# Kernel tuning notes

Measured on AMD Instinct MI355X. Metric: run time of the kernel, lower is better.

## Reference

```python
import jax, jax.numpy as jnp
import numpy as np

B, N_C, N_T, D, DF = 16, 2048, 1024, 2, 2
K, E_OBS = 16, 4
H, DH = 4, 16
F = H * DH  # 64-dim node features (embed_all output)


def setup_inputs() -> dict:
    key = jax.random.key(0)
    ks = jax.random.split(key, 16)
    r = lambda i, shape: jax.random.normal(ks[i], shape, jnp.float32) * 0.05
    d_in = E_OBS + D + DF  # obs(4) + s(2) + f(2) = 8
    return dict(
        s_ctx=jax.random.normal(ks[0], (B, N_C, D), jnp.float32),
        f_ctx=jax.random.normal(ks[1], (B, N_C, DF), jnp.float32),
        s_test=jax.random.normal(ks[2], (B, N_T, D), jnp.float32),
        emb_obs=r(3, (2, E_OBS)),
        W1=r(4, (d_in, 256)), b1=jnp.zeros((256,), jnp.float32),
        W2=r(5, (256, 128)), b2=jnp.zeros((128,), jnp.float32),
        W3=r(6, (128, F)), b3=jnp.zeros((F,), jnp.float32),
        ln_g=jnp.ones((F,), jnp.float32), ln_b=jnp.zeros((F,), jnp.float32),
        Wg=r(7, (F, F)),
        a_src=r(8, (H, DH)), a_dst=r(9, (H, DH)),
        We=r(10, (D, H)), be=jnp.zeros((H,), jnp.float32),
        H1=r(11, (F, 256)), c1=jnp.zeros((256,), jnp.float32),
        H2=r(12, (256, 64)), c2=jnp.zeros((64,), jnp.float32),
        H3=r(13, (64, 2)), c3=jnp.zeros((2,), jnp.float32),
    )


def _knn(q, ctx, k):
    # q [B,Nq,D], ctx [B,Nc,D] -> neighbor indices [B,Nq,K] and displacement edge feats [B,Nq,K,D]
    d2 = (jnp.sum(q * q, -1)[:, :, None] + jnp.sum(ctx * ctx, -1)[:, None, :]
          - 2.0 * jnp.einsum('bqd,bcd->bqc', q, ctx))
    _, idx = jax.lax.top_k(-d2, k)
    nb = jax.vmap(lambda c, i: c[i])(ctx, idx)  # gather neighbor coords per batch
    return idx, q[:, :, None, :] - nb


def _mlp3(x, W1, b1, W2, b2, W3, b3):
    x = jax.nn.gelu(x @ W1 + b1)
    x = jax.nn.gelu(x @ W2 + b2)
    return x @ W3 + b3


def _ln(x, g, b):
    mu = jnp.mean(x, -1, keepdims=True)
    v = jnp.var(x, -1, keepdims=True)
    return (x - mu) * jax.lax.rsqrt(v + 1e-6) * g + b


def reference(s_ctx, f_ctx, s_test, emb_obs, W1, b1, W2, b2, W3, b3, ln_g, ln_b,
              Wg, a_src, a_dst, We, be, H1, c1, H2, c2, H3, c3):
    # --- build kNN graph (ctx->ctx and ctx->test edges, K per receiver) ---
    s_cc, d_cc = _knn(s_ctx, s_ctx, K)
    s_ct, d_ct = _knn(s_test, s_ctx, K)
    edges = jnp.concatenate([d_cc.reshape(-1, D), d_ct.reshape(-1, D)], axis=0)  # [E, D]
    off = (jnp.arange(B) * N_C)[:, None, None]
    senders = jnp.concatenate([(s_cc + off).reshape(-1), (s_ct + off).reshape(-1)])  # [E]
    # receivers == repeat(arange(N), K): edges are grouped K-per-node in node order.

    # --- node embedding: [obs_embed | s | f] -> MLP -> LayerNorm ---
    ctx_in = jnp.concatenate([jnp.broadcast_to(emb_obs[1], (B, N_C, E_OBS)), s_ctx, f_ctx], -1)
    test_in = jnp.concatenate([jnp.broadcast_to(emb_obs[0], (B, N_T, E_OBS)), s_test,
                               jnp.zeros((B, N_T, DF), s_test.dtype)], -1)
    n_ctx = _ln(_mlp3(ctx_in, W1, b1, W2, b2, W3, b3), ln_g, ln_b)
    n_test = _ln(_mlp3(test_in, W1, b1, W2, b2, W3, b3), ln_g, ln_b)
    nodes = jnp.concatenate([n_ctx.reshape(B * N_C, F), n_test.reshape(B * N_T, F)], 0)
    N = B * (N_C + N_T)

    # --- edge-biased GAT message passing (K incoming edges per node) ---
    xp = (nodes @ Wg).reshape(N, H, DH)
    msg = xp[senders].reshape(N, K, H, DH)  # gather sender features
    sc = (jnp.einsum('nkhd,hd->nkh', msg, a_src)
          + jnp.einsum('nhd,hd->nh', xp, a_dst)[:, None, :])
    sc = jax.nn.leaky_relu(sc, 0.2) + (edges @ We + be).reshape(N, K, H)  # edge bias
    alpha = jax.nn.softmax(sc, axis=1)  # softmax over the K neighbors
    out = jnp.einsum('nkh,nkhd->nhd', alpha, msg).reshape(N, F)
    nodes = nodes + out  # residual

    # --- head on test nodes + diagonal MVN output ---
    n_t = nodes[-B * N_T:].reshape(B, N_T, F)
    o = jax.nn.gelu(n_t @ H1 + c1)
    o = jax.nn.gelu(o @ H2 + c2)
    o = o @ H3 + c3  # [B, N_t, 2]
    mean = o[..., 0:1]
    scale = jax.nn.softplus(o[..., 1:2])
    return jnp.concatenate([mean, scale], -1)
```

## Files before the change

### kernel.cpp

```cpp
#include <hip/hip_runtime.h>
#include <math.h>

#define NB 16
#define NCTX 2048
#define NTEST 1024
#define NCTX_TOT (NB*NCTX)
#define NTEST_TOT (NB*NTEST)
#define NTOT (NCTX_TOT + NTEST_TOT)

typedef _Float16 half8 __attribute__((ext_vector_type(8)));
typedef _Float16 half4 __attribute__((ext_vector_type(4)));
typedef float f32x4 __attribute__((ext_vector_type(4)));

__device__ __forceinline__ float gelu_f(float x) {
  float x3 = x * x * x;
  float y = 0.7978845608028654f * fmaf(0.044715f, x3, x);
  float e = __expf(2.0f * y);
  float th = 1.0f - 2.0f * __builtin_amdgcn_rcpf(e + 1.0f);
  return 0.5f * x * (1.0f + th);
}

__device__ __forceinline__ void fma4(float4& a, float s, float4 w) {
  a.x = fmaf(s, w.x, a.x);
  a.y = fmaf(s, w.y, a.y);
  a.z = fmaf(s, w.z, a.z);
  a.w = fmaf(s, w.w, a.w);
}

__device__ __forceinline__ float4 ldg4(const float* p) {
  return *reinterpret_cast<const float4*>(p);
}

__device__ __forceinline__ unsigned fkey(float f) {
  unsigned u = __float_as_uint(f);
  return (u & 0x80000000u) ? ~u : (u ^ 0x80000000u);
}
__device__ __forceinline__ float unfkey(unsigned k) {
  return (k & 0x80000000u) ? __uint_as_float(k ^ 0x80000000u)
                           : __uint_as_float(~k);
}

__global__ __launch_bounds__(256, 3) void knn_prep_kernel(
    const float* __restrict__ s_ctx, const float* __restrict__ s_test,
    int* __restrict__ senders,
    const float* __restrict__ W1, const float* __restrict__ b1,
    const float* __restrict__ emb,
    const float* __restrict__ W2, const float* __restrict__ W3,
    const float* __restrict__ Wg,
    const float* __restrict__ H1, const float* __restrict__ H2,
    _Float16* __restrict__ W2P, _Float16* __restrict__ W3P,
    _Float16* __restrict__ WgP,
    _Float16* __restrict__ H1P, _Float16* __restrict__ H2P,
    float* __restrict__ ctype)
{
  __shared__ __align__(16) unsigned long long sk[4][128];
  const int blk = blockIdx.x;

  if (blk < 40) {
    const int t = blk*256 + (int)threadIdx.x;
    if (t < 4096) {
      int i = t;
      int j = i >> 9, ks = (i >> 6) & 7, l = i & 63;
      int col = 16*j + (l & 15);
      int k0  = ks*32 + (l >> 4)*8;
      half8 o;
      #pragma unroll
      for (int e = 0; e < 8; ++e) o[e] = (_Float16)W2[(k0 + e)*128 + col];
      *reinterpret_cast<half8*>(&W2P[(size_t)i*8]) = o;
    } else if (t < 5120) {
      int i = t - 4096;
      int j = i >> 8, ks = (i >> 6) & 3, l = i & 63;
      int col = 16*j + (l & 15);
      int k0  = ks*32 + (l >> 4)*8;
      half8 o;
      #pragma unroll
      for (int e = 0; e < 8; ++e) o[e] = (_Float16)W3[(k0 + e)*64 + col];
      *reinterpret_cast<half8*>(&W3P[(size_t)i*8]) = o;
    } else if (t < 5632) {
      int i = t - 5120;
      int j = i >> 7, ks = (i >> 6) & 1, l = i & 63;
      int col = 16*j + (l & 15);
      int k0  = ks*32 + (l >> 4)*8;
      half8 o;
      #pragma unroll
      for (int e = 0; e < 8; ++e) o[e] = (_Float16)Wg[(k0 + e)*64 + col];
      *reinterpret_cast<half8*>(&WgP[(size_t)i*8]) = o;
    } else if (t < 7680) {
      int i = t - 5632;
      int j = i >> 7, ks = (i >> 6) & 1, l = i & 63;
      int col = 16*j + (l & 15);
      int k0  = ks*32 + (l >> 4)*8;
      half8 o;
      #pragma unroll
      for (int e = 0; e < 8; ++e) o[e] = (_Float16)H1[(k0 + e)*256 + col];
      *reinterpret_cast<half8*>(&H1P[(size_t)i*8]) = o;
    } else if (t < 9728) {
      int i = t - 7680;
      int j = i >> 9, ks = (i >> 6) & 7, l = i & 63;
      int col = 16*j + (l & 15);
      int k0  = ks*32 + (l >> 4)*8;
      half8 o;
      #pragma unroll
      for (int e = 0; e < 8; ++e) o[e] = (_Float16)H2[(k0 + e)*64 + col];
      *reinterpret_cast<half8*>(&H2P[(size_t)i*8]) = o;
    } else {
      int i = t - 9728;
      int ty = i >> 8, c = i & 255;
      float acc = b1[c];
      #pragma unroll
      for (int k = 0; k < 4; ++k) acc = fmaf(emb[ty*4 + k], W1[k*256 + c], acc);
      ctype[i] = acc;
    }
    return;
  }

  const int t    = threadIdx.x;
  const int lane = t & 63;
  const int w    = t >> 6;
  const int b0   = blk - 40;
  const int unit = (b0 & 7)*512 + (b0 >> 3);
  const int bb   = unit >> 8;
  const int q    = (unit & 255) * 4 + w;
  const int trow = bb * NTEST + q;

  const float* cb = s_ctx + (size_t)bb * NCTX * 2;
  const float qx = s_test[(size_t)trow*2];
  const float qy = s_test[(size_t)trow*2 + 1];
  const float qq = __fadd_rn(__fmul_rn(qx,qx), __fmul_rn(qy,qy));

  float2 p[32];
  #pragma unroll
  for (int it = 0; it < 32; ++it)
    p[it] = *reinterpret_cast<const float2*>(&cb[2*(it*64 + lane)]);

  float d[32];
  float mn = 3.4e38f;
  #pragma unroll
  for (int it = 0; it < 32; ++it) {
    float ss  = __fadd_rn(__fmul_rn(p[it].x,p[it].x), __fmul_rn(p[it].y,p[it].y));
    float dot = __fadd_rn(__fmul_rn(qx, p[it].x), __fmul_rn(qy, p[it].y));
    float d2  = __fsub_rn(__fadd_rn(qq, ss), __fmul_rn(2.0f, dot));
    d[it] = d2;
    mn = fminf(mn, d2);
  }

  unsigned v = fkey(mn);
  #pragma unroll
  for (int k = 2; k <= 64; k <<= 1) {
    #pragma unroll
    for (int j = k >> 1; j >= 1; j >>= 1) {
      unsigned pv = (unsigned)__shfl_xor((int)v, j);
      bool up      = ((lane & k) == 0);
      bool lowHalf = ((lane & j) == 0);
      bool keepMin = (lowHalf == up);
      unsigned mnv = v < pv ? v : pv;
      unsigned mxv = v < pv ? pv : v;
      v = keepMin ? mnv : mxv;
    }
  }
  const float Tf = unfkey((unsigned)__shfl((int)v, 15));

  int cnt = 0;
  #pragma unroll
  for (int it = 0; it < 32; ++it) cnt += (int)(d[it] <= Tf);
  int inc = cnt;
  #pragma unroll
  for (int o = 1; o < 64; o <<= 1) {
    int y = __shfl_up(inc, o);
    if (lane >= o) inc += y;
  }
  const int S = __shfl(inc, 63);
  int pos = inc - cnt;
  #pragma unroll
  for (int it = 0; it < 32; ++it) {
    if (d[it] <= Tf) {
      if (pos < 128)
        sk[w][pos] = ((unsigned long long)fkey(d[it]) << 32)
                   | (unsigned)(it*64 + lane);
      ++pos;
    }
  }

  if (S <= 32) {
    if (lane >= S && lane < 32) sk[w][lane] = ~0ULL;
    unsigned long long pm = sk[w][lane & 31];
    unsigned long long kv[32];
    #pragma unroll
    for (int j = 0; j < 32; ++j) kv[j] = sk[w][j];
    int r0 = 0;
    #pragma unroll
    for (int j = 0; j < 32; ++j)
      r0 += (int)(kv[j] < pm);
    if (lane < S && r0 < 16)
      senders[(size_t)trow*16 + r0] = bb*NCTX + (int)(pm & 0xFFFFFFFFu);
  } else if (S <= 128) {
    unsigned long long p0 = (lane      < S) ? sk[w][lane]      : ~0ULL;
    unsigned long long p1 = (lane + 64 < S) ? sk[w][lane + 64] : ~0ULL;
    int r0 = 0, r1 = 0;
    for (int j = 0; j < S; ++j) {
      unsigned long long kj = sk[w][j];
      r0 += (int)(kj < p0);
      r1 += (int)(kj < p1);
    }
    if (lane < S && r0 < 16)
      senders[(size_t)trow*16 + r0] = bb*NCTX + (int)(p0 & 0xFFFFFFFFu);
    if (lane + 64 < S && r1 < 16)
      senders[(size_t)trow*16 + r1] = bb*NCTX + (int)(p1 & 0xFFFFFFFFu);
  } else {
    if (lane == 0) {
      float dist[16]; int ind[16];
      #pragma unroll
      for (int j=0;j<16;++j){ dist[j]=3.4e38f; ind[j]=0; }
      for (int c = 0; c < NCTX; ++c) {
        float2 pp = *reinterpret_cast<const float2*>(&cb[2*c]);
        float ss  = __fadd_rn(__fmul_rn(pp.x,pp.x), __fmul_rn(pp.y,pp.y));
        float dot = __fadd_rn(__fmul_rn(qx, pp.x), __fmul_rn(qy, pp.y));
        float d2  = __fsub_rn(__fadd_rn(qq, ss), __fmul_rn(2.0f, dot));
        if (d2 < dist[15]) {
          float dj = d2; int ij = c;
          #pragma unroll
          for (int j = 0; j < 16; ++j) {
            bool sw = dj < dist[j];
            float td = dist[j]; int ti = ind[j];
            dist[j] = sw ? dj : td;  ind[j] = sw ? ij : ti;
            dj = sw ? td : dj;       ij = sw ? ti : ij;
          }
        }
      }
      for (int j = 0; j < 16; ++j)
        senders[(size_t)trow*16 + j] = bb*NCTX + ind[j];
    }
  }
}

__global__ __launch_bounds__(256, 4) void mlp_kernel(
    const float* __restrict__ s_ctx, const float* __restrict__ f_ctx,
    const float* __restrict__ s_test,
    const float* __restrict__ ctype, const float* __restrict__ W1,
    const _Float16* __restrict__ W2P, const float* __restrict__ b2,
    const _Float16* __restrict__ W3P, const float* __restrict__ b3,
    const float* __restrict__ ln_g, const float* __restrict__ ln_b,
    const _Float16* __restrict__ WgP,
    const float* __restrict__ a_src, const float* __restrict__ a_dst,
    float* __restrict__ nodes, _Float16* __restrict__ xph,
    float* __restrict__ xps, float* __restrict__ xpd)
{
  __shared__ __align__(16) char smem[34816];
  const int t    = threadIdx.x;
  const int lane = t & 63;
  const int w    = t >> 6;
  const int id   = blockIdx.x;
  char* slice = smem + w * 8704;
  _Float16* h1t  = reinterpret_cast<_Float16*>(slice);
  float (*xin)[4] = reinterpret_cast<float(*)[4]>(slice + 8448);
  _Float16* h2   = h1t;
  _Float16* nodh = h1t + 16*136;
  const int cn = lane & 15;
  const int kg = lane >> 4;
  const int m0 = (id*4 + w) * 16;
  const bool is_ctx = (m0 < NCTX_TOT);

  const _Float16* bQ2 = W2P + lane*8;
  const _Float16* bQ3 = W3P + lane*8;
  const _Float16* bQg = WgP + lane*8;

  half8 bb2[8];
  #pragma unroll
  for (int j = 0; j < 8; ++j)
    bb2[j] = *reinterpret_cast<const half8*>(bQ2 + j*4096);

  {
    int r = lane >> 2, c = lane & 3;
    int n = m0 + r;
    float v;
    if (is_ctx) v = (c < 2) ? s_ctx[2*(size_t)n + c] : f_ctx[2*(size_t)n + (c-2)];
    else { int tn = n - NCTX_TOT; v = (c < 2) ? s_test[2*(size_t)tn + c] : 0.f; }
    xin[r][c] = v;
  }

  {
    const int c0 = lane * 4;
    float4 w4 = ldg4(&W1[4*256 + c0]);
    float4 w5 = ldg4(&W1[5*256 + c0]);
    float4 w6 = ldg4(&W1[6*256 + c0]);
    float4 w7 = ldg4(&W1[7*256 + c0]);
    float4 cbv = ldg4(&ctype[(is_ctx ? 256 : 0) + c0]);
    #pragma unroll
    for (int r = 0; r < 16; ++r) {
      float4 xi = *reinterpret_cast<const float4*>(&xin[r][0]);
      float4 a = cbv;
      fma4(a, xi.x, w4); fma4(a, xi.y, w5);
      fma4(a, xi.z, w6); fma4(a, xi.w, w7);
      half4 o = { (_Float16)gelu_f(a.x), (_Float16)gelu_f(a.y),
                  (_Float16)gelu_f(a.z), (_Float16)gelu_f(a.w) };
      *reinterpret_cast<half4*>(&h1t[r*264 + c0]) = o;
    }
  }

  {
    f32x4 acc[8];
    #pragma unroll
    for (int j = 0; j < 8; ++j) {
      float bv = b2[16*j + cn];
      acc[j] = (f32x4){bv, bv, bv, bv};
    }
    const _Float16* aP = h1t + cn*264 + kg*8;
    #pragma unroll
    for (int ks = 0; ks < 8; ++ks) {
      half8 a = *reinterpret_cast<const half8*>(aP + ks*32);
      half8 bn[8];
      if (ks < 7) {
        #pragma unroll
        for (int j = 0; j < 8; ++j)
          bn[j] = *reinterpret_cast<const half8*>(bQ2 + j*4096 + (ks+1)*512);
      }
      #pragma unroll
      for (int j = 0; j < 8; ++j)
        acc[j] = __builtin_amdgcn_mfma_f32_16x16x32_f16(a, bb2[j], acc[j], 0, 0, 0);
      if (ks < 7) {
        #pragma unroll
        for (int j = 0; j < 8; ++j) bb2[j] = bn[j];
      }
    }
    #pragma unroll
    for (int j = 0; j < 8; ++j)
      #pragma unroll
      for (int r = 0; r < 4; ++r) {
        int m = kg*4 + r;
        h2[m*136 + 16*j + cn] = (_Float16)gelu_f(acc[j][r]);
      }
  }

  {
    f32x4 acc[4];
    #pragma unroll
    for (int j = 0; j < 4; ++j) {
      float bv = b3[16*j + cn];
      acc[j] = (f32x4){bv, bv, bv, bv};
    }
    const _Float16* aP = h2 + cn*136 + kg*8;
    half8 bb[4];
    #pragma unroll
    for (int j = 0; j < 4; ++j)
      bb[j] = *reinterpret_cast<const half8*>(bQ3 + j*2048);
    #pragma unroll
    for (int ks = 0; ks < 4; ++ks) {
      half8 a = *reinterpret_cast<const half8*>(aP + ks*32);
      half8 bn[4];
      if (ks < 3) {
        #pragma unroll
        for (int j = 0; j < 4; ++j)
          bn[j] = *reinterpret_cast<const half8*>(bQ3 + j*2048 + (ks+1)*512);
      }
      #pragma unroll
      for (int j = 0; j < 4; ++j)
        acc[j] = __builtin_amdgcn_mfma_f32_16x16x32_f16(a, bb[j], acc[j], 0, 0, 0);
      if (ks < 3) {
        #pragma unroll
        for (int j = 0; j < 4; ++j) bb[j] = bn[j];
      }
    }
    float gv[4], bvv[4];
    #pragma unroll
    for (int j = 0; j < 4; ++j) { gv[j] = ln_g[16*j+cn]; bvv[j] = ln_b[16*j+cn]; }
    const bool is_test = !is_ctx;
    #pragma unroll
    for (int r = 0; r < 4; ++r) {
      float sv = 0.f, sq = 0.f;
      #pragma unroll
      for (int j = 0; j < 4; ++j) {
        float v = acc[j][r];
        sv += v; sq += v*v;
      }
      #pragma unroll
      for (int o = 1; o < 16; o <<= 1) {
        sv += __shfl_xor(sv, o);
        sq += __shfl_xor(sq, o);
      }
      float mean = sv * (1.0f/64.0f);
      float var  = sq * (1.0f/64.0f) - mean*mean;
      float rstd = rsqrtf(var + 1e-6f);
      int m = kg*4 + r;
      #pragma unroll
      for (int j = 0; j < 4; ++j) {
        float v = (acc[j][r] - mean) * rstd * gv[j] + bvv[j];
        nodh[m*72 + 16*j + cn] = (_Float16)v;
        if (is_test)
          nodes[(size_t)(m0 + m)*64 + 16*j + cn] = v;
      }
    }
  }

  {
    f32x4 acc[4];
    #pragma unroll
    for (int j = 0; j < 4; ++j) acc[j] = (f32x4){0.f, 0.f, 0.f, 0.f};
    const _Float16* aP = nodh + cn*72 + kg*8;
    half8 bg0[4], bg1[4];
    #pragma unroll
    for (int j = 0; j < 4; ++j) {
      bg0[j] = *reinterpret_cast<const half8*>(bQg + j*1024);
      bg1[j] = *reinterpret_cast<const half8*>(bQg + j*1024 + 512);
    }
    half8 a0 = *reinterpret_cast<const half8*>(aP);
    half8 a1 = *reinterpret_cast<const half8*>(aP + 32);
    #pragma unroll
    for (int j = 0; j < 4; ++j)
      acc[j] = __builtin_amdgcn_mfma_f32_16x16x32_f16(a0, bg0[j], acc[j], 0, 0, 0);
    #pragma unroll
    for (int j = 0; j < 4; ++j)
      acc[j] = __builtin_amdgcn_mfma_f32_16x16x32_f16(a1, bg1[j], acc[j], 0, 0, 0);
    #pragma unroll
    for (int r = 0; r < 4; ++r) {
      int m = kg*4 + r;
      #pragma unroll
      for (int j = 0; j < 4; ++j)
        xph[(size_t)(m0 + m)*64 + 16*j + cn] = (_Float16)acc[j][r];
    }
    const float* av = is_ctx ? a_src : a_dst;
    float av0 = av[cn], av1 = av[16+cn], av2 = av[32+cn], av3 = av[48+cn];
    #pragma unroll
    for (int r = 0; r < 4; ++r) {
      float p0 = acc[0][r]*av0, p1 = acc[1][r]*av1;
      float p2 = acc[2][r]*av2, p3 = acc[3][r]*av3;
      #pragma unroll
      for (int o = 1; o < 16; o <<= 1) {
        p0 += __shfl_xor(p0, o); p1 += __shfl_xor(p1, o);
        p2 += __shfl_xor(p2, o); p3 += __shfl_xor(p3, o);
      }
      if (cn == 0) {
        int m = kg*4 + r;
        float4 v = make_float4(p0, p1, p2, p3);
        if (is_ctx)
          *reinterpret_cast<float4*>(&xps[(size_t)(m0 + m)*4]) = v;
        else
          *reinterpret_cast<float4*>(&xpd[(size_t)(m0 + m - NCTX_TOT)*4]) = v;
      }
    }
  }
}

__global__ __launch_bounds__(128, 3) void back_kernel(
    const float* __restrict__ s_ctx, const float* __restrict__ s_test,
    const _Float16* __restrict__ xph, const int* __restrict__ senders,
    const float* __restrict__ xps, const float* __restrict__ xpd,
    const float* __restrict__ We, const float* __restrict__ be,
    const float* __restrict__ nodes,
    const _Float16* __restrict__ H1P, const float* __restrict__ c1,
    const _Float16* __restrict__ H2P, const float* __restrict__ c2,
    const float* __restrict__ H3, const float* __restrict__ c3,
    float* __restrict__ outp)
{
  __shared__ __align__(16) _Float16 xinh[16*72];
  __shared__ __align__(16) _Float16 h1[16*264];
  __shared__ float pp[2][16][2];
  const int tid  = threadIdx.x;
  const int lane = tid & 63;
  const int wv   = tid >> 6;
  const int cn   = lane & 15;
  const int kg   = lane >> 4;
  const int bid  = blockIdx.x;
  const int L    = (bid & 7)*128 + (bid >> 3);
  const int row0 = L * 16;

  {
    const int h  = kg;
    const int kk = cn;
    const int hb = lane & 48;
    const float we0 = We[h], we1 = We[4+h], beh = be[h];
    for (int rr = 0; rr < 8; ++rr) {
      const int rl   = wv*8 + rr;
      const int trow = row0 + rl;
      int s = senders[(size_t)trow*16 + kk];
      s = (s < 0) ? 0 : ((s >= NCTX_TOT) ? NCTX_TOT - 1 : s);
      float pre = xps[(size_t)s*4 + h] + xpd[(size_t)trow*4 + h];
      float lr  = pre >= 0.f ? pre : 0.2f * pre;
      const float qx = s_test[(size_t)trow*2];
      const float qy = s_test[(size_t)trow*2 + 1];
      float ex = qx - s_ctx[(size_t)s*2];
      float ey = qy - s_ctx[(size_t)s*2 + 1];
      float sc = lr + fmaf(ex, we0, fmaf(ey, we1, beh));
      float mx = sc;
      #pragma unroll
      for (int o = 1; o < 16; o <<= 1) mx = fmaxf(mx, __shfl_xor(mx, o));
      float e = __expf(sc - mx);
      float sum = e;
      #pragma unroll
      for (int o = 1; o < 16; o <<= 1) sum += __shfl_xor(sum, o);
      float alpha = e / sum;
      float outv = 0.f;
      #pragma unroll
      for (int k = 0; k < 16; ++k) {
        int   sk = __shfl(s, k);
        float al = __shfl(alpha, hb + k);
        outv = fmaf(al, (float)xph[(size_t)sk*64 + lane], outv);
      }
      float xv = nodes[(size_t)(NCTX_TOT + trow)*64 + lane] + outv;
      xinh[rl*72 + lane] = (_Float16)xv;
    }
  }

  __syncthreads();

  {
    const _Float16* aP  = xinh + cn*72 + kg*8;
    const _Float16* bQ1 = H1P + lane*8;
    half8 a0 = *reinterpret_cast<const half8*>(aP);
    half8 a1 = *reinterpret_cast<const half8*>(aP + 32);
    const int g = wv;
    f32x4 acc[8];
    #pragma unroll
    for (int j = 0; j < 8; ++j) {
      float bv = c1[16*(g*8 + j) + cn];
      acc[j] = (f32x4){bv, bv, bv, bv};
    }
    half8 b0[8], b1[8];
    #pragma unroll
    for (int j = 0; j < 8; ++j) {
      b0[j] = *reinterpret_cast<const half8*>(bQ1 + ((g*8 + j)*2 + 0)*512);
      b1[j] = *reinterpret_cast<const half8*>(bQ1 + ((g*8 + j)*2 + 1)*512);
    }
    #pragma unroll
    for (int j = 0; j < 8; ++j)
      acc[j] = __builtin_amdgcn_mfma_f32_16x16x32_f16(a0, b0[j], acc[j], 0, 0, 0);
    #pragma unroll
    for (int j = 0; j < 8; ++j)
      acc[j] = __builtin_amdgcn_mfma_f32_16x16x32_f16(a1, b1[j], acc[j], 0, 0, 0);
    #pragma unroll
    for (int j = 0; j < 8; ++j)
      #pragma unroll
      for (int r = 0; r < 4; ++r)
        h1[(kg*4 + r)*264 + 16*(g*8 + j) + cn] = (_Float16)gelu_f(acc[j][r]);
  }

  __syncthreads();

  {
    f32x4 acc[2];
    #pragma unroll
    for (int j2 = 0; j2 < 2; ++j2) {
      const int j = wv*2 + j2;
      float bv = c2[16*j + cn];
      acc[j2] = (f32x4){bv, bv, bv, bv};
    }
    const _Float16* aP  = h1 + cn*264 + kg*8;
    const _Float16* bQ2 = H2P + lane*8;
    half8 bb[2];
    #pragma unroll
    for (int j2 = 0; j2 < 2; ++j2)
      bb[j2] = *reinterpret_cast<const half8*>(bQ2 + (wv*2 + j2)*4096);
    #pragma unroll
    for (int ks = 0; ks < 8; ++ks) {
      half8 a = *reinterpret_cast<const half8*>(aP + ks*32);
      half8 bn[2];
      if (ks < 7) {
        #pragma unroll
        for (int j2 = 0; j2 < 2; ++j2)
          bn[j2] = *reinterpret_cast<const half8*>(bQ2 + (wv*2 + j2)*4096 + (ks+1)*512);
      }
      #pragma unroll
      for (int j2 = 0; j2 < 2; ++j2)
        acc[j2] = __builtin_amdgcn_mfma_f32_16x16x32_f16(a, bb[j2], acc[j2], 0, 0, 0);
      if (ks < 7) {
        #pragma unroll
        for (int j2 = 0; j2 < 2; ++j2) bb[j2] = bn[j2];
      }
    }
    float h30[2], h31[2];
    #pragma unroll
    for (int j2 = 0; j2 < 2; ++j2) {
      const int j = wv*2 + j2;
      h30[j2] = H3[(16*j + cn)*2 + 0];
      h31[j2] = H3[(16*j + cn)*2 + 1];
    }
    #pragma unroll
    for (int r = 0; r < 4; ++r) {
      float p0 = 0.f, p1 = 0.f;
      #pragma unroll
      for (int j2 = 0; j2 < 2; ++j2) {
        float g = gelu_f(acc[j2][r]);
        p0 = fmaf(g, h30[j2], p0);
        p1 = fmaf(g, h31[j2], p1);
      }
      #pragma unroll
      for (int o = 1; o < 16; o <<= 1) {
        p0 += __shfl_xor(p0, o);
        p1 += __shfl_xor(p1, o);
      }
      if (cn == 0) {
        pp[wv][kg*4 + r][0] = p0;
        pp[wv][kg*4 + r][1] = p1;
      }
    }
  }

  __syncthreads();

  if (wv == 0 && lane < 16) {
    const float c30 = c3[0], c31 = c3[1];
    float m  = pp[0][lane][0] + pp[1][lane][0] + c30;
    float sa = pp[0][lane][1] + pp[1][lane][1] + c31;
    float sv = fmaxf(sa, 0.f) + log1pf(__expf(-fabsf(sa)));
    int row = row0 + lane;
    outp[(size_t)row*2 + 0] = m;
    outp[(size_t)row*2 + 1] = sv;
  }
}

extern "C" void kernel_launch(void* const* d_in, const int* in_sizes, int n_in,
                              void* d_out, int out_size, void* d_ws, size_t ws_size,
                              hipStream_t stream) {
  const float* s_ctx  = (const float*)d_in[0];
  const float* f_ctx  = (const float*)d_in[1];
  const float* s_test = (const float*)d_in[2];
  const float* emb    = (const float*)d_in[3];
  const float* W1 = (const float*)d_in[4];
  const float* b1 = (const float*)d_in[5];
  const float* W2 = (const float*)d_in[6];
  const float* b2 = (const float*)d_in[7];
  const float* W3 = (const float*)d_in[8];
  const float* b3 = (const float*)d_in[9];
  const float* ln_g = (const float*)d_in[10];
  const float* ln_b = (const float*)d_in[11];
  const float* Wg = (const float*)d_in[12];
  const float* a_src = (const float*)d_in[13];
  const float* a_dst = (const float*)d_in[14];
  const float* We = (const float*)d_in[15];
  const float* be = (const float*)d_in[16];
  const float* H1 = (const float*)d_in[17];
  const float* c1 = (const float*)d_in[18];
  const float* H2 = (const float*)d_in[19];
  const float* c2 = (const float*)d_in[20];
  const float* H3 = (const float*)d_in[21];
  const float* c3 = (const float*)d_in[22];

  float* nodes   = (float*)d_ws;
  _Float16* xph  = (_Float16*)(nodes + (size_t)NTOT*64);
  int*   senders = (int*)(xph + (size_t)NTOT*64);
  _Float16* W2P  = (_Float16*)(senders + (size_t)NTEST_TOT*16);
  _Float16* W3P  = W2P + 32768;
  _Float16* WgP  = W3P + 8192;
  _Float16* H1P  = WgP + 4096;
  _Float16* H2P  = H1P + 16384;
  float*   ctype = (float*)(H2P + 16384);
  float*   xps   = ctype + 512;
  float*   xpd   = xps + (size_t)NCTX_TOT*4;
  float* outp    = (float*)d_out;

  hipLaunchKernelGGL(knn_prep_kernel, dim3(4136), dim3(256), 0, stream,
                     s_ctx, s_test, senders,
                     W1, b1, emb, W2, W3, Wg, H1, H2,
                     W2P, W3P, WgP, H1P, H2P, ctype);
  hipLaunchKernelGGL(mlp_kernel, dim3(768), dim3(256), 0, stream,
                     s_ctx, f_ctx, s_test, ctype, W1,
                     W2P, b2, W3P, b3, ln_g, ln_b, WgP,
                     a_src, a_dst, nodes, xph, xps, xpd);
  hipLaunchKernelGGL(back_kernel, dim3(1024), dim3(128), 0, stream,
                     s_ctx, s_test, xph, senders, xps, xpd, We, be,
                     nodes, H1P, c1, H2P, c2, H3, c3, outp);
}
```

Measured before the change: 64.07 us.

## Process two row tiles per wave in MLP kernel; widen back kernel to four waves

In mlp_kernel each wave now handles two 16-row tiles, so one set of W2/W3/Wg fragments loaded from global memory feeds MFMAs for both tiles. The block drops to 128 threads, covering the same rows with half the waves. In back_kernel the block grows to 256 threads, and the H1/H2 output columns and edge rows are split across four waves instead of two. The aim is less redundant weight loading in the MLP and more parallelism in the head. The cost is higher register pressure (two accumulator sets) and lower occupancy in mlp_kernel.

```diff
diff --git a/kernel.cpp b/kernel.cpp
--- a/kernel.cpp
+++ b/kernel.cpp
@@ -233,7 +233,7 @@
   }
 }
 
-__global__ __launch_bounds__(256, 4) void mlp_kernel(
+__global__ __launch_bounds__(128, 2) void mlp_kernel(
     const float* __restrict__ s_ctx, const float* __restrict__ f_ctx,
     const float* __restrict__ s_test,
     const float* __restrict__ ctype, const float* __restrict__ W1,
@@ -250,15 +250,23 @@
   const int lane = t & 63;
   const int w    = t >> 6;
   const int id   = blockIdx.x;
-  char* slice = smem + w * 8704;
-  _Float16* h1t  = reinterpret_cast<_Float16*>(slice);
-  float (*xin)[4] = reinterpret_cast<float(*)[4]>(slice + 8448);
-  _Float16* h2   = h1t;
-  _Float16* nodh = h1t + 16*136;
-  const int cn = lane & 15;
-  const int kg = lane >> 4;
-  const int m0 = (id*4 + w) * 16;
-  const bool is_ctx = (m0 < NCTX_TOT);
+  const int cn   = lane & 15;
+  const int kg   = lane >> 4;
+
+  char* slice0 = smem + (w*2 + 0) * 8704;
+  char* slice1 = smem + (w*2 + 1) * 8704;
+  _Float16* h1t0 = reinterpret_cast<_Float16*>(slice0);
+  _Float16* h1t1 = reinterpret_cast<_Float16*>(slice1);
+  float (*xin0)[4] = reinterpret_cast<float(*)[4]>(slice0 + 8448);
+  float (*xin1)[4] = reinterpret_cast<float(*)[4]>(slice1 + 8448);
+  _Float16* h20 = h1t0;
+  _Float16* h21 = h1t1;
+  _Float16* nodh0 = h1t0 + 16*136;
+  _Float16* nodh1 = h1t1 + 16*136;
+  const int m00 = (id*4 + w*2 + 0) * 16;
+  const int m01 = (id*4 + w*2 + 1) * 16;
+  const bool isc0 = (m00 < NCTX_TOT);
+  const bool isc1 = (m01 < NCTX_TOT);
 
   const _Float16* bQ2 = W2P + lane*8;
   const _Float16* bQ3 = W3P + lane*8;
@@ -271,11 +279,18 @@
 
   {
     int r = lane >> 2, c = lane & 3;
-    int n = m0 + r;
-    float v;
-    if (is_ctx) v = (c < 2) ? s_ctx[2*(size_t)n + c] : f_ctx[2*(size_t)n + (c-2)];
-    else { int tn = n - NCTX_TOT; v = (c < 2) ? s_test[2*(size_t)tn + c] : 0.f; }
-    xin[r][c] = v;
+    {
+      int n = m00 + r; float v;
+      if (isc0) v = (c < 2) ? s_ctx[2*(size_t)n + c] : f_ctx[2*(size_t)n + (c-2)];
+      else { int tn = n - NCTX_TOT; v = (c < 2) ? s_test[2*(size_t)tn + c] : 0.f; }
+      xin0[r][c] = v;
+    }
+    {
+      int n = m01 + r; float v;
+      if (isc1) v = (c < 2) ? s_ctx[2*(size_t)n + c] : f_ctx[2*(size_t)n + (c-2)];
+      else { int tn = n - NCTX_TOT; v = (c < 2) ? s_test[2*(size_t)tn + c] : 0.f; }
+      xin1[r][c] = v;
+    }
   }
 
   {
@@ -284,30 +299,45 @@
     float4 w5 = ldg4(&W1[5*256 + c0]);
     float4 w6 = ldg4(&W1[6*256 + c0]);
     float4 w7 = ldg4(&W1[7*256 + c0]);
-    float4 cbv = ldg4(&ctype[(is_ctx ? 256 : 0) + c0]);
+    float4 cbv0 = ldg4(&ctype[(isc0 ? 256 : 0) + c0]);
+    float4 cbv1 = ldg4(&ctype[(isc1 ? 256 : 0) + c0]);
     #pragma unroll
     for (int r = 0; r < 16; ++r) {
-      float4 xi = *reinterpret_cast<const float4*>(&xin[r][0]);
-      float4 a = cbv;
-      fma4(a, xi.x, w4); fma4(a, xi.y, w5);
-      fma4(a, xi.z, w6); fma4(a, xi.w, w7);
-      half4 o = { (_Float16)gelu_f(a.x), (_Float16)gelu_f(a.y),
-                  (_Float16)gelu_f(a.z), (_Float16)gelu_f(a.w) };
-      *reinterpret_cast<half4*>(&h1t[r*264 + c0]) = o;
+      {
+        float4 xi = *reinterpret_cast<const float4*>(&xin0[r][0]);
+        float4 a = cbv0;
+        fma4(a, xi.x, w4); fma4(a, xi.y, w5);
+        fma4(a, xi.z, w6); fma4(a, xi.w, w7);
+        half4 o = { (_Float16)gelu_f(a.x), (_Float16)gelu_f(a.y),
+                    (_Float16)gelu_f(a.z), (_Float16)gelu_f(a.w) };
+        *reinterpret_cast<half4*>(&h1t0[r*264 + c0]) = o;
+      }
+      {
+        float4 xi = *reinterpret_cast<const float4*>(&xin1[r][0]);
+        float4 a = cbv1;
+        fma4(a, xi.x, w4); fma4(a, xi.y, w5);
+        fma4(a, xi.z, w6); fma4(a, xi.w, w7);
+        half4 o = { (_Float16)gelu_f(a.x), (_Float16)gelu_f(a.y),
+                    (_Float16)gelu_f(a.z), (_Float16)gelu_f(a.w) };
+        *reinterpret_cast<half4*>(&h1t1[r*264 + c0]) = o;
+      }
     }
   }
 
   {
-    f32x4 acc[8];
+    f32x4 acc0[8], acc1[8];
     #pragma unroll
     for (int j = 0; j < 8; ++j) {
       float bv = b2[16*j + cn];
-      acc[j] = (f32x4){bv, bv, bv, bv};
-    }
-    const _Float16* aP = h1t + cn*264 + kg*8;
+      acc0[j] = (f32x4){bv, bv, bv, bv};
+      acc1[j] = (f32x4){bv, bv, bv, bv};
+    }
+    const _Float16* aP0 = h1t0 + cn*264 + kg*8;
+    const _Float16* aP1 = h1t1 + cn*264 + kg*8;
     #pragma unroll
     for (int ks = 0; ks < 8; ++ks) {
-      half8 a = *reinterpret_cast<const half8*>(aP + ks*32);
+      half8 a0 = *reinterpret_cast<const half8*>(aP0 + ks*32);
+      half8 a1 = *reinterpret_cast<const half8*>(aP1 + ks*32);
       half8 bn[8];
       if (ks < 7) {
         #pragma unroll
@@ -315,8 +345,10 @@
           bn[j] = *reinterpret_cast<const half8*>(bQ2 + j*4096 + (ks+1)*512);
       }
       #pragma unroll
-      for (int j = 0; j < 8; ++j)
-        acc[j] = __builtin_amdgcn_mfma_f32_16x16x32_f16(a, bb2[j], acc[j], 0, 0, 0);
+      for (int j = 0; j < 8; ++j) {
+        acc0[j] = __builtin_amdgcn_mfma_f32_16x16x32_f16(a0, bb2[j], acc0[j], 0, 0, 0);
+        acc1[j] = __builtin_amdgcn_mfma_f32_16x16x32_f16(a1, bb2[j], acc1[j], 0, 0, 0);
+      }
       if (ks < 7) {
         #pragma unroll
         for (int j = 0; j < 8; ++j) bb2[j] = bn[j];
@@ -327,25 +359,29 @@
       #pragma unroll
       for (int r = 0; r < 4; ++r) {
         int m = kg*4 + r;
-        h2[m*136 + 16*j + cn] = (_Float16)gelu_f(acc[j][r]);
+        h20[m*136 + 16*j + cn] = (_Float16)gelu_f(acc0[j][r]);
+        h21[m*136 + 16*j + cn] = (_Float16)gelu_f(acc1[j][r]);
       }
   }
 
   {
-    f32x4 acc[4];
+    f32x4 acc0[4], acc1[4];
     #pragma unroll
     for (int j = 0; j < 4; ++j) {
       float bv = b3[16*j + cn];
-      acc[j] = (f32x4){bv, bv, bv, bv};
-    }
-    const _Float16* aP = h2 + cn*136 + kg*8;
+      acc0[j] = (f32x4){bv, bv, bv, bv};
+      acc1[j] = (f32x4){bv, bv, bv, bv};
+    }
+    const _Float16* aP0 = h20 + cn*136 + kg*8;
+    const _Float16* aP1 = h21 + cn*136 + kg*8;
     half8 bb[4];
     #pragma unroll
     for (int j = 0; j < 4; ++j)
       bb[j] = *reinterpret_cast<const half8*>(bQ3 + j*2048);
     #pragma unroll
     for (int ks = 0; ks < 4; ++ks) {
-      half8 a = *reinterpret_cast<const half8*>(aP + ks*32);
+      half8 a0 = *reinterpret_cast<const half8*>(aP0 + ks*32);
+      half8 a1 = *reinterpret_cast<const half8*>(aP1 + ks*32);
       half8 bn[4];
       if (ks < 3) {
         #pragma unroll
@@ -353,8 +389,10 @@
           bn[j] = *reinterpret_cast<const half8*>(bQ3 + j*2048 + (ks+1)*512);
       }
       #pragma unroll
-      for (int j = 0; j < 4; ++j)
-        acc[j] = __builtin_amdgcn_mfma_f32_16x16x32_f16(a, bb[j], acc[j], 0, 0, 0);
+      for (int j = 0; j < 4; ++j) {
+        acc0[j] = __builtin_amdgcn_mfma_f32_16x16x32_f16(a0, bb[j], acc0[j], 0, 0, 0);
+        acc1[j] = __builtin_amdgcn_mfma_f32_16x16x32_f16(a1, bb[j], acc1[j], 0, 0, 0);
+      }
       if (ks < 3) {
         #pragma unroll
         for (int j = 0; j < 4; ++j) bb[j] = bn[j];
@@ -363,13 +401,12 @@
     float gv[4], bvv[4];
     #pragma unroll
     for (int j = 0; j < 4; ++j) { gv[j] = ln_g[16*j+cn]; bvv[j] = ln_b[16*j+cn]; }
-    const bool is_test = !is_ctx;
     #pragma unroll
     for (int r = 0; r < 4; ++r) {
       float sv = 0.f, sq = 0.f;
       #pragma unroll
       for (int j = 0; j < 4; ++j) {
-        float v = acc[j][r];
+        float v = acc0[j][r];
         sv += v; sq += v*v;
       }
       #pragma unroll
@@ -383,64 +420,125 @@
       int m = kg*4 + r;
       #pragma unroll
       for (int j = 0; j < 4; ++j) {
-        float v = (acc[j][r] - mean) * rstd * gv[j] + bvv[j];
-        nodh[m*72 + 16*j + cn] = (_Float16)v;
-        if (is_test)
-          nodes[(size_t)(m0 + m)*64 + 16*j + cn] = v;
+        float v = (acc0[j][r] - mean) * rstd * gv[j] + bvv[j];
+        nodh0[m*72 + 16*j + cn] = (_Float16)v;
+        if (!isc0)
+          nodes[(size_t)(m00 + m)*64 + 16*j + cn] = v;
+      }
+    }
+    #pragma unroll
+    for (int r = 0; r < 4; ++r) {
+      float sv = 0.f, sq = 0.f;
+      #pragma unroll
+      for (int j = 0; j < 4; ++j) {
+        float v = acc1[j][r];
+        sv += v; sq += v*v;
+      }
+      #pragma unroll
+      for (int o = 1; o < 16; o <<= 1) {
+        sv += __shfl_xor(sv, o);
+        sq += __shfl_xor(sq, o);
+      }
+      float mean = sv * (1.0f/64.0f);
+      float var  = sq * (1.0f/64.0f) - mean*mean;
+      float rstd = rsqrtf(var + 1e-6f);
+      int m = kg*4 + r;
+      #pragma unroll
+      for (int j = 0; j < 4; ++j) {
+        float v = (acc1[j][r] - mean) * rstd * gv[j] + bvv[j];
+        nodh1[m*72 + 16*j + cn] = (_Float16)v;
+        if (!isc1)
+          nodes[(size_t)(m01 + m)*64 + 16*j + cn] = v;
       }
     }
   }
 
   {
-    f32x4 acc[4];
-    #pragma unroll
-    for (int j = 0; j < 4; ++j) acc[j] = (f32x4){0.f, 0.f, 0.f, 0.f};
-    const _Float16* aP = nodh + cn*72 + kg*8;
+    f32x4 acc0[4], acc1[4];
+    #pragma unroll
+    for (int j = 0; j < 4; ++j) {
+      acc0[j] = (f32x4){0.f, 0.f, 0.f, 0.f};
+      acc1[j] = (f32x4){0.f, 0.f, 0.f, 0.f};
+    }
+    const _Float16* aP0 = nodh0 + cn*72 + kg*8;
+    const _Float16* aP1 = nodh1 + cn*72 + kg*8;
     half8 bg0[4], bg1[4];
     #pragma unroll
     for (int j = 0; j < 4; ++j) {
       bg0[j] = *reinterpret_cast<const half8*>(bQg + j*1024);
       bg1[j] = *reinterpret_cast<const half8*>(bQg + j*1024 + 512);
     }
-    half8 a0 = *reinterpret_cast<const half8*>(aP);
-    half8 a1 = *reinterpret_cast<const half8*>(aP + 32);
-    #pragma unroll
-    for (int j = 0; j < 4; ++j)
-      acc[j] = __builtin_amdgcn_mfma_f32_16x16x32_f16(a0, bg0[j], acc[j], 0, 0, 0);
-    #pragma unroll
-    for (int j = 0; j < 4; ++j)
-      acc[j] = __builtin_amdgcn_mfma_f32_16x16x32_f16(a1, bg1[j], acc[j], 0, 0, 0);
+    half8 a00 = *reinterpret_cast<const half8*>(aP0);
+    half8 a01 = *reinterpret_cast<const half8*>(aP0 + 32);
+    half8 a10 = *reinterpret_cast<const half8*>(aP1);
+    half8 a11 = *reinterpret_cast<const half8*>(aP1 + 32);
+    #pragma unroll
+    for (int j = 0; j < 4; ++j) {
+      acc0[j] = __builtin_amdgcn_mfma_f32_16x16x32_f16(a00, bg0[j], acc0[j], 0, 0, 0);
+      acc1[j] = __builtin_amdgcn_mfma_f32_16x16x32_f16(a10, bg0[j], acc1[j], 0, 0, 0);
+    }
+    #pragma unroll
+    for (int j = 0; j < 4; ++j) {
+      acc0[j] = __builtin_amdgcn_mfma_f32_16x16x32_f16(a01, bg1[j], acc0[j], 0, 0, 0);
+      acc1[j] = __builtin_amdgcn_mfma_f32_16x16x32_f16(a11, bg1[j], acc1[j], 0, 0, 0);
+    }
     #pragma unroll
     for (int r = 0; r < 4; ++r) {
       int m = kg*4 + r;
       #pragma unroll
-      for (int j = 0; j < 4; ++j)
-        xph[(size_t)(m0 + m)*64 + 16*j + cn] = (_Float16)acc[j][r];
-    }
-    const float* av = is_ctx ? a_src : a_dst;
-    float av0 = av[cn], av1 = av[16+cn], av2 = av[32+cn], av3 = av[48+cn];
-    #pragma unroll
-    for (int r = 0; r < 4; ++r) {
-      float p0 = acc[0][r]*av0, p1 = acc[1][r]*av1;
-      float p2 = acc[2][r]*av2, p3 = acc[3][r]*av3;
-      #pragma unroll
-      for (int o = 1; o < 16; o <<= 1) {
-        p0 += __shfl_xor(p0, o); p1 += __shfl_xor(p1, o);
-        p2 += __shfl_xor(p2, o); p3 += __shfl_xor(p3, o);
-      }
-      if (cn == 0) {
-        int m = kg*4 + r;
-        float4 v = make_float4(p0, p1, p2, p3);
-        if (is_ctx)
-          *reinterpret_cast<float4*>(&xps[(size_t)(m0 + m)*4]) = v;
-        else
-          *reinterpret_cast<float4*>(&xpd[(size_t)(m0 + m - NCTX_TOT)*4]) = v;
-      }
-    }
-  }
-}
-
-__global__ __launch_bounds__(128, 3) void back_kernel(
+      for (int j = 0; j < 4; ++j) {
+        xph[(size_t)(m00 + m)*64 + 16*j + cn] = (_Float16)acc0[j][r];
+        xph[(size_t)(m01 + m)*64 + 16*j + cn] = (_Float16)acc1[j][r];
+      }
+    }
+    {
+      const float* av = isc0 ? a_src : a_dst;
+      float av0 = av[cn], av1 = av[16+cn], av2 = av[32+cn], av3 = av[48+cn];
+      #pragma unroll
+      for (int r = 0; r < 4; ++r) {
+        float p0 = acc0[0][r]*av0, p1 = acc0[1][r]*av1;
+        float p2 = acc0[2][r]*av2, p3 = acc0[3][r]*av3;
+        #pragma unroll
+        for (int o = 1; o < 16; o <<= 1) {
+          p0 += __shfl_xor(p0, o); p1 += __shfl_xor(p1, o);
+          p2 += __shfl_xor(p2, o); p3 += __shfl_xor(p3, o);
+        }
+        if (cn == 0) {
+          int m = kg*4 + r;
+          float4 v = make_float4(p0, p1, p2, p3);
+          if (isc0)
+            *reinterpret_cast<float4*>(&xps[(size_t)(m00 + m)*4]) = v;
+          else
+            *reinterpret_cast<float4*>(&xpd[(size_t)(m00 + m - NCTX_TOT)*4]) = v;
+        }
+      }
+    }
+    {
+      const float* av = isc1 ? a_src : a_dst;
+      float av0 = av[cn], av1 = av[16+cn], av2 = av[32+cn], av3 = av[48+cn];
+      #pragma unroll
+      for (int r = 0; r < 4; ++r) {
+        float p0 = acc1[0][r]*av0, p1 = acc1[1][r]*av1;
+        float p2 = acc1[2][r]*av2, p3 = acc1[3][r]*av3;
+        #pragma unroll
+        for (int o = 1; o < 16; o <<= 1) {
+          p0 += __shfl_xor(p0, o); p1 += __shfl_xor(p1, o);
+          p2 += __shfl_xor(p2, o); p3 += __shfl_xor(p3, o);
+        }
+        if (cn == 0) {
+          int m = kg*4 + r;
+          float4 v = make_float4(p0, p1, p2, p3);
+          if (isc1)
+            *reinterpret_cast<float4*>(&xps[(size_t)(m01 + m)*4]) = v;
+          else
+            *reinterpret_cast<float4*>(&xpd[(size_t)(m01 + m - NCTX_TOT)*4]) = v;
+        }
+      }
+    }
+  }
+}
+
+__global__ __launch_bounds__(256, 4) void back_kernel(
     const float* __restrict__ s_ctx, const float* __restrict__ s_test,
     const _Float16* __restrict__ xph, const int* __restrict__ senders,
     const float* __restrict__ xps, const float* __restrict__ xpd,
@@ -453,7 +551,7 @@
 {
   __shared__ __align__(16) _Float16 xinh[16*72];
   __shared__ __align__(16) _Float16 h1[16*264];
-  __shared__ float pp[2][16][2];
+  __shared__ float pp[4][16][2];
   const int tid  = threadIdx.x;
   const int lane = tid & 63;
   const int wv   = tid >> 6;
@@ -468,8 +566,8 @@
     const int kk = cn;
     const int hb = lane & 48;
     const float we0 = We[h], we1 = We[4+h], beh = be[h];
-    for (int rr = 0; rr < 8; ++rr) {
-      const int rl   = wv*8 + rr;
+    for (int rr = 0; rr < 4; ++rr) {
+      const int rl   = wv*4 + rr;
       const int trow = row0 + rl;
       int s = senders[(size_t)trow*16 + kk];
       s = (s < 0) ? 0 : ((s >= NCTX_TOT) ? NCTX_TOT - 1 : s);
@@ -507,81 +605,62 @@
     const _Float16* bQ1 = H1P + lane*8;
     half8 a0 = *reinterpret_cast<const half8*>(aP);
     half8 a1 = *reinterpret_cast<const half8*>(aP + 32);
-    const int g = wv;
-    f32x4 acc[8];
-    #pragma unroll
-    for (int j = 0; j < 8; ++j) {
-      float bv = c1[16*(g*8 + j) + cn];
-      acc[j] = (f32x4){bv, bv, bv, bv};
-    }
-    half8 b0[8], b1[8];
-    #pragma unroll
-    for (int j = 0; j < 8; ++j) {
-      b0[j] = *reinterpret_cast<const half8*>(bQ1 + ((g*8 + j)*2 + 0)*512);
-      b1[j] = *reinterpret_cast<const half8*>(bQ1 + ((g*8 + j)*2 + 1)*512);
-    }
-    #pragma unroll
-    for (int j = 0; j < 8; ++j)
-      acc[j] = __builtin_amdgcn_mfma_f32_16x16x32_f16(a0, b0[j], acc[j], 0, 0, 0);
-    #pragma unroll
-    for (int j = 0; j < 8; ++j)
-      acc[j] = __builtin_amdgcn_mfma_f32_16x16x32_f16(a1, b1[j], acc[j], 0, 0, 0);
-    #pragma unroll
-    for (int j = 0; j < 8; ++j)
+    f32x4 acc[4];
+    #pragma unroll
+    for (int j2 = 0; j2 < 4; ++j2) {
+      const int jj = wv*4 + j2;
+      float bv = c1[16*jj + cn];
+      acc[j2] = (f32x4){bv, bv, bv, bv};
+    }
+    half8 b0[4], b1[4];
+    #pragma unroll
+    for (int j2 = 0; j2 < 4; ++j2) {
+      const int jj = wv*4 + j2;
+      b0[j2] = *reinterpret_cast<const half8*>(bQ1 + (jj*2 + 0)*512);
+      b1[j2] = *reinterpret_cast<const half8*>(bQ1 + (jj*2 + 1)*512);
+    }
+    #pragma unroll
+    for (int j2 = 0; j2 < 4; ++j2)
+      acc[j2] = __builtin_amdgcn_mfma_f32_16x16x32_f16(a0, b0[j2], acc[j2], 0, 0, 0);
+    #pragma unroll
+    for (int j2 = 0; j2 < 4; ++j2)
+      acc[j2] = __builtin_amdgcn_mfma_f32_16x16x32_f16(a1, b1[j2], acc[j2], 0, 0, 0);
+    #pragma unroll
+    for (int j2 = 0; j2 < 4; ++j2) {
+      const int jj = wv*4 + j2;
       #pragma unroll
       for (int r = 0; r < 4; ++r)
-        h1[(kg*4 + r)*264 + 16*(g*8 + j) + cn] = (_Float16)gelu_f(acc[j][r]);
+        h1[(kg*4 + r)*264 + 16*jj + cn] = (_Float16)gelu_f(acc[j2][r]);
+    }
   }
 
   __syncthreads();
 
   {
-    f32x4 acc[2];
-    #pragma unroll
-    for (int j2 = 0; j2 < 2; ++j2) {
-      const int j = wv*2 + j2;
-      float bv = c2[16*j + cn];
-      acc[j2] = (f32x4){bv, bv, bv, bv};
+    f32x4 acc;
+    {
+      float bv = c2[16*wv + cn];
+      acc = (f32x4){bv, bv, bv, bv};
     }
     const _Float16* aP  = h1 + cn*264 + kg*8;
     const _Float16* bQ2 = H2P + lane*8;
-    half8 bb[2];
-    #pragma unroll
-    for (int j2 = 0; j2 < 2; ++j2)
-      bb[j2] = *reinterpret_cast<const half8*>(bQ2 + (wv*2 + j2)*4096);
+    half8 bb = *reinterpret_cast<const half8*>(bQ2 + wv*4096);
     #pragma unroll
     for (int ks = 0; ks < 8; ++ks) {
       half8 a = *reinterpret_cast<const half8*>(aP + ks*32);
-      half8 bn[2];
-      if (ks < 7) {
-        #pragma unroll
-        for (int j2 = 0; j2 < 2; ++j2)
-          bn[j2] = *reinterpret_cast<const half8*>(bQ2 + (wv*2 + j2)*4096 + (ks+1)*512);
-      }
-      #pragma unroll
-      for (int j2 = 0; j2 < 2; ++j2)
-        acc[j2] = __builtin_amdgcn_mfma_f32_16x16x32_f16(a, bb[j2], acc[j2], 0, 0, 0);
-      if (ks < 7) {
-        #pragma unroll
-        for (int j2 = 0; j2 < 2; ++j2) bb[j2] = bn[j2];
-      }
-    }
-    float h30[2], h31[2];
-    #pragma unroll
-    for (int j2 = 0; j2 < 2; ++j2) {
-      const int j = wv*2 + j2;
-      h30[j2] = H3[(16*j + cn)*2 + 0];
-      h31[j2] = H3[(16*j + cn)*2 + 1];
-    }
+      half8 bn;
+      if (ks < 7)
+        bn = *reinterpret_cast<const half8*>(bQ2 + wv*4096 + (ks+1)*512);
+      acc = __builtin_amdgcn_mfma_f32_16x16x32_f16(a, bb, acc, 0, 0, 0);
+      if (ks < 7) bb = bn;
+    }
+    float h30 = H3[(16*wv + cn)*2 + 0];
+    float h31 = H3[(16*wv + cn)*2 + 1];
     #pragma unroll
     for (int r = 0; r < 4; ++r) {
-      float p0 = 0.f, p1 = 0.f;
-      #pragma unroll
-      for (int j2 = 0; j2 < 2; ++j2) {
-        float g = gelu_f(acc[j2][r]);
-        p0 = fmaf(g, h30[j2], p0);
-        p1 = fmaf(g, h31[j2], p1);
-      }
+      float g  = gelu_f(acc[r]);
+      float p0 = g * h30;
+      float p1 = g * h31;
       #pragma unroll
       for (int o = 1; o < 16; o <<= 1) {
         p0 += __shfl_xor(p0, o);
@@ -598,8 +677,10 @@
 
   if (wv == 0 && lane < 16) {
     const float c30 = c3[0], c31 = c3[1];
-    float m  = pp[0][lane][0] + pp[1][lane][0] + c30;
-    float sa = pp[0][lane][1] + pp[1][lane][1] + c31;
+    float m  = pp[0][lane][0] + pp[1][lane][0] + pp[2][lane][0]
+             + pp[3][lane][0] + c30;
+    float sa = pp[0][lane][1] + pp[1][lane][1] + pp[2][lane][1]
+             + pp[3][lane][1] + c31;
     float sv = fmaxf(sa, 0.f) + log1pf(__expf(-fabsf(sa)));
     int row = row0 + lane;
     outp[(size_t)row*2 + 0] = m;
@@ -651,11 +732,11 @@
                      s_ctx, s_test, senders,
                      W1, b1, emb, W2, W3, Wg, H1, H2,
                      W2P, W3P, WgP, H1P, H2P, ctype);
-  hipLaunchKernelGGL(mlp_kernel, dim3(768), dim3(256), 0, stream,
+  hipLaunchKernelGGL(mlp_kernel, dim3(768), dim3(128), 0, stream,
                      s_ctx, f_ctx, s_test, ctype, W1,
                      W2P, b2, W3P, b3, ln_g, ln_b, WgP,
                      a_src, a_dst, nodes, xph, xps, xpd);
-  hipLaunchKernelGGL(back_kernel, dim3(1024), dim3(128), 0, stream,
+  hipLaunchKernelGGL(back_kernel, dim3(1024), dim3(256), 0, stream,
                      s_ctx, s_test, xph, senders, xps, xpd, We, be,
                      nodes, H1P, c1, H2P, c2, H3, c3, outp);
 }
```

Measured after the change: 69.13 us. +7.9%, slower.
